# Kernel tuning notes

Measured on AMD Instinct MI355X. Metric: run time of the kernel, lower is better.

Reference implementation:

```python
import jax, jax.numpy as jnp
import numpy as np

B, S, D = 8, 2048, 256


def setup_inputs() -> dict:
    key = jax.random.key(0)
    ks = jax.random.split(key, 8)
    nodes = jax.random.normal(ks[0], (B, S, D), dtype=jnp.float32)
    mask = jax.random.randint(ks[1], (B, S), 0, 2, dtype=jnp.int32)
    # ensure at least one unmasked position per row to avoid all--inf softmax
    mask = mask.at[:, 0].set(1)
    scale = 1.0 / np.sqrt(D)
    Wq = jax.random.normal(ks[2], (D, D), dtype=jnp.float32) * scale
    bq = jnp.zeros((D,), dtype=jnp.float32)
    Wk = jax.random.normal(ks[3], (D, D), dtype=jnp.float32) * scale
    bk = jnp.zeros((D,), dtype=jnp.float32)
    Wv = jax.random.normal(ks[4], (D, D), dtype=jnp.float32) * scale
    bv = jnp.zeros((D,), dtype=jnp.float32)
    return {"nodes": nodes, "mask": mask, "Wq": Wq, "bq": bq,
            "Wk": Wk, "bk": bk, "Wv": Wv, "bv": bv}


def reference(nodes, mask, Wq, bq, Wk, bk, Wv, bv):
    # Linear layers: x @ W.T + b (torch nn.Linear convention)
    q = jnp.einsum('bsd,ed->bse', nodes, Wq) + bq   # [B,S,D]
    k = jnp.einsum('bsd,ed->bse', nodes, Wk) + bk
    v = jnp.einsum('bsd,ed->bse', nodes, Wv) + bv
    d = k.shape[-1]
    scores = jnp.einsum('bqd,bkd->bqk', q, k) / jnp.sqrt(jnp.float32(d))  # [B,S,S]
    # mask[b, j] == 0 masks key column j for every query row
    scores = jnp.where(mask[:, None, :] != 0, scores, -jnp.inf)
    attn = jax.nn.softmax(scores, axis=-1)           # [B,S,S]
    weighted = jnp.einsum('bqk,bkd->bqd', attn, v)   # [B,S,D]
    return jnp.mean(weighted, axis=1)                # [B,D]
```

## Files before the change

### kernel.cpp

```cpp
#include <hip/hip_runtime.h>
#include <hip/hip_bf16.h>
#include <stdint.h>


typedef short short8 __attribute__((ext_vector_type(8)));
typedef float floatx4 __attribute__((ext_vector_type(4)));

#define MFMA16(a, b, c) __builtin_amdgcn_mfma_f32_16x16x32_bf16((a), (b), (c), 0, 0, 0)

static __device__ __forceinline__ unsigned short f2bf(float f) {
    union { float f; unsigned u; } v; v.f = f;
    unsigned r = v.u + 0x7fffu + ((v.u >> 16) & 1u);
    return (unsigned short)(r >> 16);
}
static __device__ __forceinline__ float bf2f(unsigned short h) {
    union { unsigned u; float f; } v; v.u = ((unsigned)h) << 16;
    return v.f;
}

__global__ __launch_bounds__(256) void k_convert(
    const float* __restrict__ nodes, const float* __restrict__ Wq,
    const float* __restrict__ Wk, const float* __restrict__ Wv,
    unsigned short* __restrict__ nbf, unsigned short* __restrict__ wbf)
{
    int unit = blockIdx.x * 256 + threadIdx.x;
    const float* src;
    unsigned short* dst;
    int off;
    if (unit < 524288) {
        src = nodes; dst = nbf; off = unit * 8;
    } else {
        int j = (unit - 524288) * 8;
        int m = j >> 16;
        int r = j & 65535;
        src = (m == 0) ? Wq : (m == 1 ? Wk : Wv);
        dst = wbf + m * 65536;
        off = r;
    }
    float4 a = *(const float4*)(src + off);
    float4 b = *(const float4*)(src + off + 4);
    short8 o;
    o[0] = f2bf(a.x); o[1] = f2bf(a.y); o[2] = f2bf(a.z); o[3] = f2bf(a.w);
    o[4] = f2bf(b.x); o[5] = f2bf(b.y); o[6] = f2bf(b.z); o[7] = f2bf(b.w);
    *(short8*)(dst + off) = o;
}

__global__ __launch_bounds__(256) void k_proj2(
    const unsigned short* __restrict__ nbf,
    const unsigned short* __restrict__ wbf,
    const float* __restrict__ bq, const float* __restrict__ bk,
    const float* __restrict__ bv,
    unsigned short* __restrict__ qb, unsigned short* __restrict__ kb,
    unsigned short* __restrict__ vb)
{
    __shared__ unsigned short As[128 * 64];
    __shared__ unsigned short Bs[128 * 64];
    int tid = threadIdx.x, lane = tid & 63, wave = tid >> 6;
    int wm = wave & 1, wn = wave >> 1;
    int l15 = lane & 15, quad = lane >> 4;
    int mBase = blockIdx.x * 128;
    int nBase = blockIdx.y * 128;
    int z = blockIdx.z;
    const unsigned short* W = wbf + z * 65536;

    floatx4 acc[4][4] = {};

    int srow[4], scol[4];
#pragma unroll
    for (int i = 0; i < 4; ++i) {
        int p = i * 256 + tid;
        srow[i] = p >> 3;
        scol[i] = (p & 7) ^ (srow[i] & 7);
    }

    for (int kc = 0; kc < 256; kc += 64) {
#pragma unroll
        for (int i = 0; i < 4; ++i) {
            int p = i * 256 + tid;
            *(short8*)(&As[p * 8]) =
                *(const short8*)(nbf + (mBase + srow[i]) * 256 + kc + scol[i] * 8);
            *(short8*)(&Bs[p * 8]) =
                *(const short8*)(W + (nBase + srow[i]) * 256 + kc + scol[i] * 8);
        }
        __syncthreads();
#pragma unroll
        for (int ks = 0; ks < 2; ++ks) {
            int c8 = ks * 4 + quad;
            short8 af[4], bfr[4];
#pragma unroll
            for (int i = 0; i < 4; ++i) {
                int row = wm * 64 + i * 16 + l15;
                af[i] = *(const short8*)(&As[(row * 8 + (c8 ^ (row & 7))) * 8]);
            }
#pragma unroll
            for (int i = 0; i < 4; ++i) {
                int row = wn * 64 + i * 16 + l15;
                bfr[i] = *(const short8*)(&Bs[(row * 8 + (c8 ^ (row & 7))) * 8]);
            }
#pragma unroll
            for (int mi = 0; mi < 4; ++mi)
#pragma unroll
                for (int ni = 0; ni < 4; ++ni)
                    acc[mi][ni] = MFMA16(af[mi], bfr[ni], acc[mi][ni]);
        }
        __syncthreads();
    }

    const float* bias = (z == 0) ? bq : (z == 1 ? bk : bv);
    unsigned short* out = (z == 0) ? qb : (z == 1 ? kb : vb);
    float scale = (z == 0) ? 0.0625f : 1.0f;
#pragma unroll
    for (int mi = 0; mi < 4; ++mi)
#pragma unroll
        for (int ni = 0; ni < 4; ++ni) {
            int col = nBase + wn * 64 + ni * 16 + l15;
            float bval = bias[col];
#pragma unroll
            for (int r = 0; r < 4; ++r) {
                int row = mBase + wm * 64 + mi * 16 + quad * 4 + r;
                out[row * 256 + col] = f2bf((acc[mi][ni][r] + bval) * scale);
            }
        }
}

#define LDSW 264

template <bool STORE_P>
__global__ __launch_bounds__(256) void k_pass1(
    const unsigned short* __restrict__ qb, const unsigned short* __restrict__ kb,
    const int* __restrict__ mask, float* __restrict__ lsum_g,
    unsigned short* __restrict__ pbuf)
{
    __shared__ unsigned short kt[64 * LDSW];
    __shared__ float mf[64];
    int tid = threadIdx.x, lane = tid & 63, wave = tid >> 6;
    int l15 = lane & 15, quad = lane >> 4;
    int b = blockIdx.z;
    int qBase = blockIdx.x * 128 + wave * 32;
    int kStart = blockIdx.y * 512;
    _Float16* P = (_Float16*)pbuf;

    short8 qf[2][8];
#pragma unroll
    for (int mi = 0; mi < 2; ++mi)
#pragma unroll
        for (int ks = 0; ks < 8; ++ks)
            qf[mi][ks] = *(const short8*)(qb + (b * 2048 + qBase + mi * 16 + l15) * 256 + ks * 32 + quad * 8);

    float ls[2][4] = {};
    for (int kc = kStart; kc < kStart + 512; kc += 64) {
#pragma unroll
        for (int u = tid; u < 2048; u += 256) {
            int row = u >> 5, cu = u & 31;
            *(uint4*)(&kt[row * LDSW + cu * 8]) = *(const uint4*)(kb + (b * 2048 + kc) * 256 + u * 8);
        }
        if (tid < 64) mf[tid] = mask[b * 2048 + kc + tid] ? 0.0f : -1e30f;
        __syncthreads();
#pragma unroll
        for (int nt = 0; nt < 4; ++nt) {
            short8 kf[8];
            const unsigned short* base = &kt[(nt * 16 + l15) * LDSW + quad * 8];
#pragma unroll
            for (int ks = 0; ks < 8; ++ks) kf[ks] = *(const short8*)(base + ks * 32);
            floatx4 acc[2] = {};
#pragma unroll
            for (int ks = 0; ks < 8; ++ks) {
                acc[0] = MFMA16(qf[0][ks], kf[ks], acc[0]);
                acc[1] = MFMA16(qf[1][ks], kf[ks], acc[1]);
            }
            float bv = mf[nt * 16 + l15];
#pragma unroll
            for (int mi = 0; mi < 2; ++mi)
#pragma unroll
                for (int r = 0; r < 4; ++r) {
                    float e = __expf(acc[mi][r] + bv);
                    ls[mi][r] += e;
                    if (STORE_P) {
                        int q = qBase + mi * 16 + quad * 4 + r;
                        P[(b * 2048 + q) * 2048 + kc + nt * 16 + l15] = (_Float16)e;
                    }
                }
        }
        __syncthreads();
    }
#pragma unroll
    for (int mi = 0; mi < 2; ++mi)
#pragma unroll
        for (int r = 0; r < 4; ++r) {
            float v = ls[mi][r];
            v += __shfl_xor(v, 1); v += __shfl_xor(v, 2);
            v += __shfl_xor(v, 4); v += __shfl_xor(v, 8);
            if (l15 == 0)
                atomicAdd(&lsum_g[b * 2048 + qBase + mi * 16 + quad * 4 + r], v);
        }
}

__global__ __launch_bounds__(256) void k_wred(
    const unsigned short* __restrict__ pbuf, const float* __restrict__ lsum_g,
    float* __restrict__ wsum_g)
{
    int b = blockIdx.z;
    int k = (blockIdx.x * 256 + threadIdx.x) * 2;
    int q0 = blockIdx.y * 128;
    const unsigned short* P = pbuf;
    float a0 = 0.f, a1 = 0.f;
#pragma unroll 8
    for (int q = q0; q < q0 + 128; ++q) {
        float li = 1.0f / lsum_g[b * 2048 + q];
        union { unsigned u; _Float16 h[2]; } v;
        v.u = *(const unsigned*)(P + (b * 2048 + q) * 2048 + k);
        a0 += (float)v.h[0] * li;
        a1 += (float)v.h[1] * li;
    }
    atomicAdd(&wsum_g[b * 2048 + k], a0);
    atomicAdd(&wsum_g[b * 2048 + k + 1], a1);
}

__global__ __launch_bounds__(256) void k_pass2(
    const unsigned short* __restrict__ qb, const unsigned short* __restrict__ kb,
    const int* __restrict__ mask, const float* __restrict__ lsum_g,
    float* __restrict__ wsum_g)
{
    __shared__ unsigned short kt[64 * LDSW];
    __shared__ float mf[64];
    int tid = threadIdx.x, lane = tid & 63, wave = tid >> 6;
    int l15 = lane & 15, quad = lane >> 4;
    int b = blockIdx.z;
    int qBase = blockIdx.x * 128 + wave * 32;
    int kStart = blockIdx.y * 512;

    short8 qf[2][8];
    float linv[2][4];
#pragma unroll
    for (int mi = 0; mi < 2; ++mi) {
#pragma unroll
        for (int ks = 0; ks < 8; ++ks)
            qf[mi][ks] = *(const short8*)(qb + (b * 2048 + qBase + mi * 16 + l15) * 256 + ks * 32 + quad * 8);
#pragma unroll
        for (int r = 0; r < 4; ++r)
            linv[mi][r] = 1.0f / lsum_g[b * 2048 + qBase + mi * 16 + quad * 4 + r];
    }

    for (int kc = kStart; kc < kStart + 512; kc += 64) {
#pragma unroll
        for (int u = tid; u < 2048; u += 256) {
            int row = u >> 5, cu = u & 31;
            *(uint4*)(&kt[row * LDSW + cu * 8]) = *(const uint4*)(kb + (b * 2048 + kc) * 256 + u * 8);
        }
        if (tid < 64) mf[tid] = mask[b * 2048 + kc + tid] ? 1.0f : 0.0f;
        __syncthreads();
#pragma unroll
        for (int nt = 0; nt < 4; ++nt) {
            short8 kf[8];
            const unsigned short* base = &kt[(nt * 16 + l15) * LDSW + quad * 8];
#pragma unroll
            for (int ks = 0; ks < 8; ++ks) kf[ks] = *(const short8*)(base + ks * 32);
            floatx4 acc[2] = {};
#pragma unroll
            for (int ks = 0; ks < 8; ++ks) {
                acc[0] = MFMA16(qf[0][ks], kf[ks], acc[0]);
                acc[1] = MFMA16(qf[1][ks], kf[ks], acc[1]);
            }
            float mv = mf[nt * 16 + l15];
            float part = 0.f;
#pragma unroll
            for (int mi = 0; mi < 2; ++mi)
#pragma unroll
                for (int r = 0; r < 4; ++r)
                    part += mv * __expf(fminf(acc[mi][r], 30.f)) * linv[mi][r];
            part += __shfl_xor(part, 16);
            part += __shfl_xor(part, 32);
            if (lane < 16)
                atomicAdd(&wsum_g[b * 2048 + kc + nt * 16 + lane], part);
        }
        __syncthreads();
    }
}

__global__ __launch_bounds__(256) void k_out(
    const float* __restrict__ wsum_g, const unsigned short* __restrict__ vb,
    float* __restrict__ outp)
{
    int b = blockIdx.y;
    int d = threadIdx.x;
    int k0 = blockIdx.x * 128;
    float acc = 0.f;
#pragma unroll 4
    for (int k = k0; k < k0 + 128; ++k) {
        float wv = wsum_g[b * 2048 + k];
        acc += wv * bf2f(vb[(b * 2048 + k) * 256 + d]);
    }
    atomicAdd(&outp[b * 256 + d], acc * (1.0f / 2048.0f));
}

extern "C" void kernel_launch(void* const* d_in, const int* in_sizes, int n_in,
                              void* d_out, int out_size, void* d_ws, size_t ws_size,
                              hipStream_t stream)
{
    const float* nodes = (const float*)d_in[0];
    const int*   mask  = (const int*)d_in[1];
    const float* Wq    = (const float*)d_in[2];
    const float* bq    = (const float*)d_in[3];
    const float* Wk    = (const float*)d_in[4];
    const float* bk    = (const float*)d_in[5];
    const float* Wv    = (const float*)d_in[6];
    const float* bv    = (const float*)d_in[7];
    float* out = (float*)d_out;

    unsigned short* qb  = (unsigned short*)d_ws;
    unsigned short* kb  = qb + 4194304;
    unsigned short* vb  = kb + 4194304;
    float* lsum = (float*)(vb + 4194304);
    float* wsum = lsum + 16384;
    unsigned short* X   = (unsigned short*)(wsum + 16384);
    unsigned short* nbf = X;
    unsigned short* wbf = X + 4194304;
    unsigned short* pbuf = X;

    bool useP = ws_size >= 92500000;

    hipMemsetAsync(lsum, 0, 16384 * sizeof(float), stream);
    hipMemsetAsync(wsum, 0, 16384 * sizeof(float), stream);
    hipMemsetAsync(d_out, 0, 2048 * sizeof(float), stream);

    k_convert<<<2144, 256, 0, stream>>>(nodes, Wq, Wk, Wv, nbf, wbf);
    k_proj2<<<dim3(128, 2, 3), 256, 0, stream>>>(nbf, wbf, bq, bk, bv, qb, kb, vb);
    if (useP) {
        k_pass1<true><<<dim3(16, 4, 8), 256, 0, stream>>>(qb, kb, mask, lsum, pbuf);
        k_wred<<<dim3(4, 16, 8), 256, 0, stream>>>(pbuf, lsum, wsum);
    } else {
        k_pass1<false><<<dim3(16, 4, 8), 256, 0, stream>>>(qb, kb, mask, lsum, pbuf);
        k_pass2<<<dim3(16, 4, 8), 256, 0, stream>>>(qb, kb, mask, lsum, wsum);
    }
    k_out<<<dim3(16, 8), 256, 0, stream>>>(wsum, vb, out);
}
```

Baseline: 155.9 us.

## Store P in MFMA-tile layout, XOR-swizzle K in LDS, rewrite column reduction

The score kernel now writes exp values as contiguous 16-byte per-lane fragments in an MFMA-tile-ordered buffer instead of scattered 2-byte stores, and the K tile in LDS uses an XOR swizzle instead of padding. The key range per block is halved to launch twice as many blocks. The column-sum kernel is rewritten to read the tiled layout, with per-query inverse sums cached in LDS and a shuffle reduction before the atomic add. The aim is to remove uncoalesced P stores and raise occupancy, at the cost of a custom layout that both kernels must agree on.

```diff
diff --git a/kernel.cpp b/kernel.cpp
--- a/kernel.cpp
+++ b/kernel.cpp
@@ -123,22 +123,19 @@
         }
 }
 
-#define LDSW 264
-
 template <bool STORE_P>
 __global__ __launch_bounds__(256) void k_pass1(
     const unsigned short* __restrict__ qb, const unsigned short* __restrict__ kb,
     const int* __restrict__ mask, float* __restrict__ lsum_g,
     unsigned short* __restrict__ pbuf)
 {
-    __shared__ unsigned short kt[64 * LDSW];
+    __shared__ unsigned short kt[64 * 32 * 8];
     __shared__ float mf[64];
     int tid = threadIdx.x, lane = tid & 63, wave = tid >> 6;
     int l15 = lane & 15, quad = lane >> 4;
     int b = blockIdx.z;
     int qBase = blockIdx.x * 128 + wave * 32;
-    int kStart = blockIdx.y * 512;
-    _Float16* P = (_Float16*)pbuf;
+    int kStart = blockIdx.y * 256;
 
     short8 qf[2][8];
 #pragma unroll
@@ -148,38 +145,47 @@
             qf[mi][ks] = *(const short8*)(qb + (b * 2048 + qBase + mi * 16 + l15) * 256 + ks * 32 + quad * 8);
 
     float ls[2][4] = {};
-    for (int kc = kStart; kc < kStart + 512; kc += 64) {
+    for (int kc = kStart; kc < kStart + 256; kc += 64) {
 #pragma unroll
         for (int u = tid; u < 2048; u += 256) {
             int row = u >> 5, cu = u & 31;
-            *(uint4*)(&kt[row * LDSW + cu * 8]) = *(const uint4*)(kb + (b * 2048 + kc) * 256 + u * 8);
+            int slot = row * 32 + (cu ^ (row & 7));
+            *(uint4*)(&kt[slot * 8]) = *(const uint4*)(kb + (b * 2048 + kc) * 256 + u * 8);
         }
         if (tid < 64) mf[tid] = mask[b * 2048 + kc + tid] ? 0.0f : -1e30f;
         __syncthreads();
 #pragma unroll
         for (int nt = 0; nt < 4; ++nt) {
+            int row = nt * 16 + l15;
             short8 kf[8];
-            const unsigned short* base = &kt[(nt * 16 + l15) * LDSW + quad * 8];
-#pragma unroll
-            for (int ks = 0; ks < 8; ++ks) kf[ks] = *(const short8*)(base + ks * 32);
+#pragma unroll
+            for (int ks = 0; ks < 8; ++ks) {
+                int c8 = ks * 4 + quad;
+                kf[ks] = *(const short8*)(&kt[(row * 32 + (c8 ^ (row & 7))) * 8]);
+            }
             floatx4 acc[2] = {};
 #pragma unroll
             for (int ks = 0; ks < 8; ++ks) {
                 acc[0] = MFMA16(qf[0][ks], kf[ks], acc[0]);
                 acc[1] = MFMA16(qf[1][ks], kf[ks], acc[1]);
             }
-            float bv = mf[nt * 16 + l15];
+            float bvv = mf[row];
+            short8 hh;
 #pragma unroll
             for (int mi = 0; mi < 2; ++mi)
 #pragma unroll
                 for (int r = 0; r < 4; ++r) {
-                    float e = __expf(acc[mi][r] + bv);
+                    float e = __expf(acc[mi][r] + bvv);
                     ls[mi][r] += e;
                     if (STORE_P) {
-                        int q = qBase + mi * 16 + quad * 4 + r;
-                        P[(b * 2048 + q) * 2048 + kc + nt * 16 + l15] = (_Float16)e;
+                        union { _Float16 h; short s; } u; u.h = (_Float16)e;
+                        hh[mi * 4 + r] = u.s;
                     }
                 }
+            if (STORE_P) {
+                size_t tileIdx = ((((size_t)b * 16 + blockIdx.x) * 4 + wave) * 32 + (kc >> 6)) * 4 + nt;
+                *(short8*)(pbuf + tileIdx * 512 + lane * 8) = hh;
+            }
         }
         __syncthreads();
     }
@@ -195,27 +201,43 @@
         }
 }
 
-__global__ __launch_bounds__(256) void k_wred(
+__global__ __launch_bounds__(512) void k_wred2(
     const unsigned short* __restrict__ pbuf, const float* __restrict__ lsum_g,
     float* __restrict__ wsum_g)
 {
-    int b = blockIdx.z;
-    int k = (blockIdx.x * 256 + threadIdx.x) * 2;
-    int q0 = blockIdx.y * 128;
-    const unsigned short* P = pbuf;
-    float a0 = 0.f, a1 = 0.f;
-#pragma unroll 8
-    for (int q = q0; q < q0 + 128; ++q) {
-        float li = 1.0f / lsum_g[b * 2048 + q];
-        union { unsigned u; _Float16 h[2]; } v;
-        v.u = *(const unsigned*)(P + (b * 2048 + q) * 2048 + k);
-        a0 += (float)v.h[0] * li;
-        a1 += (float)v.h[1] * li;
-    }
-    atomicAdd(&wsum_g[b * 2048 + k], a0);
-    atomicAdd(&wsum_g[b * 2048 + k + 1], a1);
-}
-
+    __shared__ float linv_s[2048];
+    int tid = threadIdx.x, lane = tid & 63, wave = tid >> 6;
+    int l15 = lane & 15, quad = lane >> 4;
+    int b = blockIdx.y, kc = blockIdx.x;
+    int nt = wave & 3;
+    int qg0 = (wave >> 2) * 32;
+
+    for (int idx = tid; idx < 2048; idx += 512) {
+        int qg = idx >> 5, qd = (idx >> 3) & 3, j = idx & 7;
+        int q = qg * 32 + (j >> 2) * 16 + qd * 4 + (j & 3);
+        linv_s[idx] = 1.0f / lsum_g[b * 2048 + q];
+    }
+    __syncthreads();
+
+    float acc = 0.f;
+#pragma unroll 4
+    for (int qg = qg0; qg < qg0 + 32; ++qg) {
+        size_t tileIdx = ((((size_t)b * 16 + (qg >> 2)) * 4 + (qg & 3)) * 32 + kc) * 4 + nt;
+        short8 hv = *(const short8*)(pbuf + tileIdx * 512 + lane * 8);
+        const float* lv = &linv_s[(qg * 4 + quad) * 8];
+#pragma unroll
+        for (int j = 0; j < 8; ++j) {
+            union { short s; _Float16 h; } u; u.s = hv[j];
+            acc += (float)u.h * lv[j];
+        }
+    }
+    acc += __shfl_xor(acc, 16);
+    acc += __shfl_xor(acc, 32);
+    if (lane < 16)
+        atomicAdd(&wsum_g[b * 2048 + kc * 64 + nt * 16 + l15], acc);
+}
+
+#define LDSW 264
 __global__ __launch_bounds__(256) void k_pass2(
     const unsigned short* __restrict__ qb, const unsigned short* __restrict__ kb,
     const int* __restrict__ mask, const float* __restrict__ lsum_g,
@@ -326,10 +348,10 @@
     k_convert<<<2144, 256, 0, stream>>>(nodes, Wq, Wk, Wv, nbf, wbf);
     k_proj2<<<dim3(128, 2, 3), 256, 0, stream>>>(nbf, wbf, bq, bk, bv, qb, kb, vb);
     if (useP) {
-        k_pass1<true><<<dim3(16, 4, 8), 256, 0, stream>>>(qb, kb, mask, lsum, pbuf);
-        k_wred<<<dim3(4, 16, 8), 256, 0, stream>>>(pbuf, lsum, wsum);
+        k_pass1<true><<<dim3(16, 8, 8), 256, 0, stream>>>(qb, kb, mask, lsum, pbuf);
+        k_wred2<<<dim3(32, 8), 512, 0, stream>>>(pbuf, lsum, wsum);
     } else {
-        k_pass1<false><<<dim3(16, 4, 8), 256, 0, stream>>>(qb, kb, mask, lsum, pbuf);
+        k_pass1<false><<<dim3(16, 8, 8), 256, 0, stream>>>(qb, kb, mask, lsum, pbuf);
         k_pass2<<<dim3(16, 4, 8), 256, 0, stream>>>(qb, kb, mask, lsum, wsum);
     }
     k_out<<<dim3(16, 8), 256, 0, stream>>>(wsum, vb, out);
```

After: 163.1 us. 1.05x slower.

## Fuse fp32-to-bf16 conversion into projection and restructure attention with tiled P layout

Applied to the files above, without the earlier changes.

Removes the separate conversion kernel by converting fp32 inputs to bf16 inside the projection GEMM's shared-memory staging. Rewrites the score pass so each wave keeps its K tile in registers and streams Q rows, storing exp-scores in an MFMA-fragment-tiled fp16 layout with vectorized 16-byte writes. The scattered per-element 2-byte stores of the old layout go away. A new reduction kernel reads that tiled layout with vector loads and per-block cached inverse row sums. The workspace-size fallback path is dropped, so the P buffer is always used, and lsum now takes more atomics per query row.

```diff
diff --git a/kernel.cpp b/kernel.cpp
--- a/kernel.cpp
+++ b/kernel.cpp
@@ -17,37 +17,17 @@
     union { unsigned u; float f; } v; v.u = ((unsigned)h) << 16;
     return v.f;
 }
-
-__global__ __launch_bounds__(256) void k_convert(
-    const float* __restrict__ nodes, const float* __restrict__ Wq,
-    const float* __restrict__ Wk, const float* __restrict__ Wv,
-    unsigned short* __restrict__ nbf, unsigned short* __restrict__ wbf)
-{
-    int unit = blockIdx.x * 256 + threadIdx.x;
-    const float* src;
-    unsigned short* dst;
-    int off;
-    if (unit < 524288) {
-        src = nodes; dst = nbf; off = unit * 8;
-    } else {
-        int j = (unit - 524288) * 8;
-        int m = j >> 16;
-        int r = j & 65535;
-        src = (m == 0) ? Wq : (m == 1 ? Wk : Wv);
-        dst = wbf + m * 65536;
-        off = r;
-    }
-    float4 a = *(const float4*)(src + off);
-    float4 b = *(const float4*)(src + off + 4);
+static __device__ __forceinline__ short8 cvt8(float4 a, float4 b) {
     short8 o;
     o[0] = f2bf(a.x); o[1] = f2bf(a.y); o[2] = f2bf(a.z); o[3] = f2bf(a.w);
     o[4] = f2bf(b.x); o[5] = f2bf(b.y); o[6] = f2bf(b.z); o[7] = f2bf(b.w);
-    *(short8*)(dst + off) = o;
-}
-
-__global__ __launch_bounds__(256) void k_proj2(
-    const unsigned short* __restrict__ nbf,
-    const unsigned short* __restrict__ wbf,
+    return o;
+}
+
+__global__ __launch_bounds__(256) void k_proj3(
+    const float* __restrict__ nodes,
+    const float* __restrict__ Wq, const float* __restrict__ Wk,
+    const float* __restrict__ Wv,
     const float* __restrict__ bq, const float* __restrict__ bk,
     const float* __restrict__ bv,
     unsigned short* __restrict__ qb, unsigned short* __restrict__ kb,
@@ -61,7 +41,7 @@
     int mBase = blockIdx.x * 128;
     int nBase = blockIdx.y * 128;
     int z = blockIdx.z;
-    const unsigned short* W = wbf + z * 65536;
+    const float* W = (z == 0) ? Wq : (z == 1 ? Wk : Wv);
 
     floatx4 acc[4][4] = {};
 
@@ -77,10 +57,10 @@
 #pragma unroll
         for (int i = 0; i < 4; ++i) {
             int p = i * 256 + tid;
-            *(short8*)(&As[p * 8]) =
-                *(const short8*)(nbf + (mBase + srow[i]) * 256 + kc + scol[i] * 8);
-            *(short8*)(&Bs[p * 8]) =
-                *(const short8*)(W + (nBase + srow[i]) * 256 + kc + scol[i] * 8);
+            const float* ap = nodes + (mBase + srow[i]) * 256 + kc + scol[i] * 8;
+            const float* bp = W + (nBase + srow[i]) * 256 + kc + scol[i] * 8;
+            *(short8*)(&As[p * 8]) = cvt8(*(const float4*)ap, *(const float4*)(ap + 4));
+            *(short8*)(&Bs[p * 8]) = cvt8(*(const float4*)bp, *(const float4*)(bp + 4));
         }
         __syncthreads();
 #pragma unroll
@@ -123,158 +103,123 @@
         }
 }
 
-#define LDSW 264
-
-template <bool STORE_P>
-__global__ __launch_bounds__(256) void k_pass1(
+__global__ __launch_bounds__(256, 2) void k_attn(
     const unsigned short* __restrict__ qb, const unsigned short* __restrict__ kb,
     const int* __restrict__ mask, float* __restrict__ lsum_g,
     unsigned short* __restrict__ pbuf)
 {
-    __shared__ unsigned short kt[64 * LDSW];
-    __shared__ float mf[64];
     int tid = threadIdx.x, lane = tid & 63, wave = tid >> 6;
     int l15 = lane & 15, quad = lane >> 4;
     int b = blockIdx.z;
-    int qBase = blockIdx.x * 128 + wave * 32;
-    int kStart = blockIdx.y * 512;
-    _Float16* P = (_Float16*)pbuf;
-
-    short8 qf[2][8];
-#pragma unroll
-    for (int mi = 0; mi < 2; ++mi)
+    int kbase = blockIdx.x * 128 + wave * 32;
+    int qs = blockIdx.y * 256;
+
+    short8 kf[2][8];
+    float mb[2];
+#pragma unroll
+    for (int nt = 0; nt < 2; ++nt) {
+        int krow = b * 2048 + kbase + nt * 16 + l15;
 #pragma unroll
         for (int ks = 0; ks < 8; ++ks)
-            qf[mi][ks] = *(const short8*)(qb + (b * 2048 + qBase + mi * 16 + l15) * 256 + ks * 32 + quad * 8);
-
-    float ls[2][4] = {};
-    for (int kc = kStart; kc < kStart + 512; kc += 64) {
-#pragma unroll
-        for (int u = tid; u < 2048; u += 256) {
-            int row = u >> 5, cu = u & 31;
-            *(uint4*)(&kt[row * LDSW + cu * 8]) = *(const uint4*)(kb + (b * 2048 + kc) * 256 + u * 8);
-        }
-        if (tid < 64) mf[tid] = mask[b * 2048 + kc + tid] ? 0.0f : -1e30f;
-        __syncthreads();
-#pragma unroll
-        for (int nt = 0; nt < 4; ++nt) {
-            short8 kf[8];
-            const unsigned short* base = &kt[(nt * 16 + l15) * LDSW + quad * 8];
-#pragma unroll
-            for (int ks = 0; ks < 8; ++ks) kf[ks] = *(const short8*)(base + ks * 32);
-            floatx4 acc[2] = {};
-#pragma unroll
-            for (int ks = 0; ks < 8; ++ks) {
-                acc[0] = MFMA16(qf[0][ks], kf[ks], acc[0]);
-                acc[1] = MFMA16(qf[1][ks], kf[ks], acc[1]);
-            }
-            float bv = mf[nt * 16 + l15];
+            kf[nt][ks] = *(const short8*)(kb + krow * 256 + ks * 32 + quad * 8);
+        mb[nt] = mask[b * 2048 + kbase + nt * 16 + l15] ? 0.0f : -1e30f;
+    }
+
+    for (int qc = 0; qc < 8; ++qc) {
+        int qBase = qs + qc * 32;
+        short8 af[2][8];
+#pragma unroll
+        for (int mi = 0; mi < 2; ++mi) {
+            int qrow = b * 2048 + qBase + mi * 16 + l15;
+#pragma unroll
+            for (int ks = 0; ks < 8; ++ks)
+                af[mi][ks] = *(const short8*)(qb + qrow * 256 + ks * 32 + quad * 8);
+        }
+        floatx4 acc[2][2] = {};
+#pragma unroll
+        for (int ks = 0; ks < 8; ++ks) {
+            acc[0][0] = MFMA16(af[0][ks], kf[0][ks], acc[0][0]);
+            acc[0][1] = MFMA16(af[0][ks], kf[1][ks], acc[0][1]);
+            acc[1][0] = MFMA16(af[1][ks], kf[0][ks], acc[1][0]);
+            acc[1][1] = MFMA16(af[1][ks], kf[1][ks], acc[1][1]);
+        }
+        float e[2][2][4];
+#pragma unroll
+        for (int mi = 0; mi < 2; ++mi)
+#pragma unroll
+            for (int nt = 0; nt < 2; ++nt)
+#pragma unroll
+                for (int r = 0; r < 4; ++r)
+                    e[mi][nt][r] = __expf(acc[mi][nt][r] + mb[nt]);
+
+        int qcg = blockIdx.y * 8 + qc;
+#pragma unroll
+        for (int nt = 0; nt < 2; ++nt) {
+            short8 hh;
 #pragma unroll
             for (int mi = 0; mi < 2; ++mi)
 #pragma unroll
                 for (int r = 0; r < 4; ++r) {
-                    float e = __expf(acc[mi][r] + bv);
-                    ls[mi][r] += e;
-                    if (STORE_P) {
-                        int q = qBase + mi * 16 + quad * 4 + r;
-                        P[(b * 2048 + q) * 2048 + kc + nt * 16 + l15] = (_Float16)e;
-                    }
+                    union { _Float16 h; short s; } u;
+                    u.h = (_Float16)e[mi][nt][r];
+                    hh[mi * 4 + r] = u.s;
                 }
-        }
-        __syncthreads();
-    }
-#pragma unroll
-    for (int mi = 0; mi < 2; ++mi)
-#pragma unroll
-        for (int r = 0; r < 4; ++r) {
-            float v = ls[mi][r];
-            v += __shfl_xor(v, 1); v += __shfl_xor(v, 2);
-            v += __shfl_xor(v, 4); v += __shfl_xor(v, 8);
-            if (l15 == 0)
-                atomicAdd(&lsum_g[b * 2048 + qBase + mi * 16 + quad * 4 + r], v);
-        }
-}
-
-__global__ __launch_bounds__(256) void k_wred(
+            int ktile = blockIdx.x * 8 + wave * 2 + nt;
+            size_t off = ((((size_t)b * 128 + ktile) * 64 + qcg) * 64 + lane) * 8;
+            *(short8*)(pbuf + off) = hh;
+        }
+#pragma unroll
+        for (int mi = 0; mi < 2; ++mi)
+#pragma unroll
+            for (int r = 0; r < 4; ++r) {
+                float v = e[mi][0][r] + e[mi][1][r];
+                v += __shfl_xor(v, 1); v += __shfl_xor(v, 2);
+                v += __shfl_xor(v, 4); v += __shfl_xor(v, 8);
+                if (l15 == 0)
+                    atomicAdd(&lsum_g[b * 2048 + qBase + mi * 16 + quad * 4 + r], v);
+            }
+    }
+}
+
+__global__ __launch_bounds__(512) void k_wred3(
     const unsigned short* __restrict__ pbuf, const float* __restrict__ lsum_g,
     float* __restrict__ wsum_g)
 {
-    int b = blockIdx.z;
-    int k = (blockIdx.x * 256 + threadIdx.x) * 2;
-    int q0 = blockIdx.y * 128;
-    const unsigned short* P = pbuf;
-    float a0 = 0.f, a1 = 0.f;
-#pragma unroll 8
-    for (int q = q0; q < q0 + 128; ++q) {
-        float li = 1.0f / lsum_g[b * 2048 + q];
-        union { unsigned u; _Float16 h[2]; } v;
-        v.u = *(const unsigned*)(P + (b * 2048 + q) * 2048 + k);
-        a0 += (float)v.h[0] * li;
-        a1 += (float)v.h[1] * li;
-    }
-    atomicAdd(&wsum_g[b * 2048 + k], a0);
-    atomicAdd(&wsum_g[b * 2048 + k + 1], a1);
-}
-
-__global__ __launch_bounds__(256) void k_pass2(
-    const unsigned short* __restrict__ qb, const unsigned short* __restrict__ kb,
-    const int* __restrict__ mask, const float* __restrict__ lsum_g,
-    float* __restrict__ wsum_g)
-{
-    __shared__ unsigned short kt[64 * LDSW];
-    __shared__ float mf[64];
+    __shared__ float linv_p[2048];
     int tid = threadIdx.x, lane = tid & 63, wave = tid >> 6;
     int l15 = lane & 15, quad = lane >> 4;
     int b = blockIdx.z;
-    int qBase = blockIdx.x * 128 + wave * 32;
-    int kStart = blockIdx.y * 512;
-
-    short8 qf[2][8];
-    float linv[2][4];
-#pragma unroll
-    for (int mi = 0; mi < 2; ++mi) {
-#pragma unroll
-        for (int ks = 0; ks < 8; ++ks)
-            qf[mi][ks] = *(const short8*)(qb + (b * 2048 + qBase + mi * 16 + l15) * 256 + ks * 32 + quad * 8);
-#pragma unroll
-        for (int r = 0; r < 4; ++r)
-            linv[mi][r] = 1.0f / lsum_g[b * 2048 + qBase + mi * 16 + quad * 4 + r];
-    }
-
-    for (int kc = kStart; kc < kStart + 512; kc += 64) {
-#pragma unroll
-        for (int u = tid; u < 2048; u += 256) {
-            int row = u >> 5, cu = u & 31;
-            *(uint4*)(&kt[row * LDSW + cu * 8]) = *(const uint4*)(kb + (b * 2048 + kc) * 256 + u * 8);
-        }
-        if (tid < 64) mf[tid] = mask[b * 2048 + kc + tid] ? 1.0f : 0.0f;
-        __syncthreads();
-#pragma unroll
-        for (int nt = 0; nt < 4; ++nt) {
-            short8 kf[8];
-            const unsigned short* base = &kt[(nt * 16 + l15) * LDSW + quad * 8];
-#pragma unroll
-            for (int ks = 0; ks < 8; ++ks) kf[ks] = *(const short8*)(base + ks * 32);
-            floatx4 acc[2] = {};
-#pragma unroll
-            for (int ks = 0; ks < 8; ++ks) {
-                acc[0] = MFMA16(qf[0][ks], kf[ks], acc[0]);
-                acc[1] = MFMA16(qf[1][ks], kf[ks], acc[1]);
-            }
-            float mv = mf[nt * 16 + l15];
-            float part = 0.f;
-#pragma unroll
-            for (int mi = 0; mi < 2; ++mi)
-#pragma unroll
-                for (int r = 0; r < 4; ++r)
-                    part += mv * __expf(fminf(acc[mi][r], 30.f)) * linv[mi][r];
-            part += __shfl_xor(part, 16);
-            part += __shfl_xor(part, 32);
-            if (lane < 16)
-                atomicAdd(&wsum_g[b * 2048 + kc + nt * 16 + lane], part);
-        }
-        __syncthreads();
-    }
+    int ktile = blockIdx.y * 8 + wave;
+
+#pragma unroll
+    for (int i = 0; i < 4; ++i) {
+        int idx = i * 512 + tid;
+        int qcg = idx >> 5, qd = (idx >> 3) & 3, j = idx & 7;
+        int q = qcg * 32 + (j >> 2) * 16 + qd * 4 + (j & 3);
+        linv_p[idx] = 1.0f / lsum_g[b * 2048 + q];
+    }
+    __syncthreads();
+
+    int qcg0 = blockIdx.x * 32;
+    float acc = 0.f;
+#pragma unroll 4
+    for (int qcg = qcg0; qcg < qcg0 + 32; ++qcg) {
+        size_t off = ((((size_t)b * 128 + ktile) * 64 + qcg) * 64 + lane) * 8;
+        short8 pv = *(const short8*)(pbuf + off);
+        const float* lv = &linv_p[(qcg * 4 + quad) * 8];
+        floatx4 l0 = *(const floatx4*)lv;
+        floatx4 l1 = *(const floatx4*)(lv + 4);
+#pragma unroll
+        for (int j = 0; j < 4; ++j) {
+            union { short s; _Float16 h; } u0, u1;
+            u0.s = pv[j]; u1.s = pv[4 + j];
+            acc += (float)u0.h * l0[j] + (float)u1.h * l1[j];
+        }
+    }
+    acc += __shfl_xor(acc, 16);
+    acc += __shfl_xor(acc, 32);
+    if (lane < 16)
+        atomicAdd(&wsum_g[b * 2048 + ktile * 16 + l15], acc);
 }
 
 __global__ __launch_bounds__(256) void k_out(
@@ -312,25 +257,15 @@
     unsigned short* vb  = kb + 4194304;
     float* lsum = (float*)(vb + 4194304);
     float* wsum = lsum + 16384;
-    unsigned short* X   = (unsigned short*)(wsum + 16384);
-    unsigned short* nbf = X;
-    unsigned short* wbf = X + 4194304;
-    unsigned short* pbuf = X;
-
-    bool useP = ws_size >= 92500000;
+    unsigned short* pbuf = (unsigned short*)(wsum + 16384);
 
     hipMemsetAsync(lsum, 0, 16384 * sizeof(float), stream);
     hipMemsetAsync(wsum, 0, 16384 * sizeof(float), stream);
     hipMemsetAsync(d_out, 0, 2048 * sizeof(float), stream);
 
-    k_convert<<<2144, 256, 0, stream>>>(nodes, Wq, Wk, Wv, nbf, wbf);
-    k_proj2<<<dim3(128, 2, 3), 256, 0, stream>>>(nbf, wbf, bq, bk, bv, qb, kb, vb);
-    if (useP) {
-        k_pass1<true><<<dim3(16, 4, 8), 256, 0, stream>>>(qb, kb, mask, lsum, pbuf);
-        k_wred<<<dim3(4, 16, 8), 256, 0, stream>>>(pbuf, lsum, wsum);
-    } else {
-        k_pass1<false><<<dim3(16, 4, 8), 256, 0, stream>>>(qb, kb, mask, lsum, pbuf);
-        k_pass2<<<dim3(16, 4, 8), 256, 0, stream>>>(qb, kb, mask, lsum, wsum);
-    }
+    k_proj3<<<dim3(128, 2, 3), 256, 0, stream>>>(nodes, Wq, Wk, Wv, bq, bk, bv,
+                                                 qb, kb, vb);
+    k_attn<<<dim3(16, 8, 8), 256, 0, stream>>>(qb, kb, mask, lsum, pbuf);
+    k_wred3<<<dim3(2, 16, 8), 512, 0, stream>>>(pbuf, lsum, wsum);
     k_out<<<dim3(16, 8), 256, 0, stream>>>(wsum, vb, out);
 }
```

New measurement: 194.9 us. 1.25x slower.

## Compact unmasked keys and fuse bf16 conversion into projection

Applied to the files above, without the earlier changes.

Adds a per-batch compaction kernel that gathers the indices of unmasked keys, and the two attention passes now iterate only over that compacted key list, skipping the fully masked columns. The fp32-to-bf16 conversion moves inside the projection GEMM's shared-memory load, so the separate conversion kernel and its scratch buffer go away. The P-buffer store/reduce path is dropped in favour of always recomputing scores in pass 2. Keys are gathered indirectly into an XOR-swizzled LDS layout, and the grid is widened to 8 key-slices that stride over the compacted range.

```diff
diff --git a/kernel.cpp b/kernel.cpp
--- a/kernel.cpp
+++ b/kernel.cpp
@@ -17,37 +17,33 @@
     union { unsigned u; float f; } v; v.u = ((unsigned)h) << 16;
     return v.f;
 }
-
-__global__ __launch_bounds__(256) void k_convert(
-    const float* __restrict__ nodes, const float* __restrict__ Wq,
-    const float* __restrict__ Wk, const float* __restrict__ Wv,
-    unsigned short* __restrict__ nbf, unsigned short* __restrict__ wbf)
-{
-    int unit = blockIdx.x * 256 + threadIdx.x;
-    const float* src;
-    unsigned short* dst;
-    int off;
-    if (unit < 524288) {
-        src = nodes; dst = nbf; off = unit * 8;
-    } else {
-        int j = (unit - 524288) * 8;
-        int m = j >> 16;
-        int r = j & 65535;
-        src = (m == 0) ? Wq : (m == 1 ? Wk : Wv);
-        dst = wbf + m * 65536;
-        off = r;
-    }
-    float4 a = *(const float4*)(src + off);
-    float4 b = *(const float4*)(src + off + 4);
+static __device__ __forceinline__ short8 cvt8(float4 a, float4 b) {
     short8 o;
     o[0] = f2bf(a.x); o[1] = f2bf(a.y); o[2] = f2bf(a.z); o[3] = f2bf(a.w);
     o[4] = f2bf(b.x); o[5] = f2bf(b.y); o[6] = f2bf(b.z); o[7] = f2bf(b.w);
-    *(short8*)(dst + off) = o;
-}
-
-__global__ __launch_bounds__(256) void k_proj2(
-    const unsigned short* __restrict__ nbf,
-    const unsigned short* __restrict__ wbf,
+    return o;
+}
+
+__global__ __launch_bounds__(64) void k_compact(
+    const int* __restrict__ mask, int* __restrict__ cidx, int* __restrict__ cnt)
+{
+    int b = blockIdx.x, lane = threadIdx.x;
+    int base = 0;
+    for (int c = 0; c < 2048; c += 64) {
+        int m = mask[b * 2048 + c + lane];
+        unsigned long long bal = __ballot(m != 0);
+        int pre = __popcll(bal & ((1ull << lane) - 1ull));
+        if (m) cidx[b * 2048 + base + pre] = c + lane;
+        base += __popcll(bal);
+    }
+    if (lane == 0) cnt[b] = base;
+    for (int i = base + lane; i < 2048; i += 64) cidx[b * 2048 + i] = 0;
+}
+
+__global__ __launch_bounds__(256) void k_proj3(
+    const float* __restrict__ nodes,
+    const float* __restrict__ Wq, const float* __restrict__ Wk,
+    const float* __restrict__ Wv,
     const float* __restrict__ bq, const float* __restrict__ bk,
     const float* __restrict__ bv,
     unsigned short* __restrict__ qb, unsigned short* __restrict__ kb,
@@ -61,7 +57,7 @@
     int mBase = blockIdx.x * 128;
     int nBase = blockIdx.y * 128;
     int z = blockIdx.z;
-    const unsigned short* W = wbf + z * 65536;
+    const float* W = (z == 0) ? Wq : (z == 1 ? Wk : Wv);
 
     floatx4 acc[4][4] = {};
 
@@ -77,10 +73,10 @@
 #pragma unroll
         for (int i = 0; i < 4; ++i) {
             int p = i * 256 + tid;
-            *(short8*)(&As[p * 8]) =
-                *(const short8*)(nbf + (mBase + srow[i]) * 256 + kc + scol[i] * 8);
-            *(short8*)(&Bs[p * 8]) =
-                *(const short8*)(W + (nBase + srow[i]) * 256 + kc + scol[i] * 8);
+            const float* ap = nodes + (mBase + srow[i]) * 256 + kc + scol[i] * 8;
+            const float* bp = W + (nBase + srow[i]) * 256 + kc + scol[i] * 8;
+            *(short8*)(&As[p * 8]) = cvt8(*(const float4*)ap, *(const float4*)(ap + 4));
+            *(short8*)(&Bs[p * 8]) = cvt8(*(const float4*)bp, *(const float4*)(bp + 4));
         }
         __syncthreads();
 #pragma unroll
@@ -123,22 +119,19 @@
         }
 }
 
-#define LDSW 264
-
-template <bool STORE_P>
-__global__ __launch_bounds__(256) void k_pass1(
+__global__ __launch_bounds__(256) void k_pass1c(
     const unsigned short* __restrict__ qb, const unsigned short* __restrict__ kb,
-    const int* __restrict__ mask, float* __restrict__ lsum_g,
-    unsigned short* __restrict__ pbuf)
-{
-    __shared__ unsigned short kt[64 * LDSW];
+    const int* __restrict__ cidx, const int* __restrict__ cnt_g,
+    float* __restrict__ lsum_g)
+{
+    __shared__ unsigned short kt[64 * 32 * 8];
     __shared__ float mf[64];
     int tid = threadIdx.x, lane = tid & 63, wave = tid >> 6;
     int l15 = lane & 15, quad = lane >> 4;
     int b = blockIdx.z;
     int qBase = blockIdx.x * 128 + wave * 32;
-    int kStart = blockIdx.y * 512;
-    _Float16* P = (_Float16*)pbuf;
+    int cnt = cnt_g[b];
+    int cntPad = (cnt + 63) & ~63;
 
     short8 qf[2][8];
 #pragma unroll
@@ -148,38 +141,37 @@
             qf[mi][ks] = *(const short8*)(qb + (b * 2048 + qBase + mi * 16 + l15) * 256 + ks * 32 + quad * 8);
 
     float ls[2][4] = {};
-    for (int kc = kStart; kc < kStart + 512; kc += 64) {
+    for (int kc = blockIdx.y * 64; kc < cntPad; kc += 512) {
 #pragma unroll
         for (int u = tid; u < 2048; u += 256) {
             int row = u >> 5, cu = u & 31;
-            *(uint4*)(&kt[row * LDSW + cu * 8]) = *(const uint4*)(kb + (b * 2048 + kc) * 256 + u * 8);
-        }
-        if (tid < 64) mf[tid] = mask[b * 2048 + kc + tid] ? 0.0f : -1e30f;
+            int krow = cidx[b * 2048 + kc + row];
+            int slot = row * 32 + (cu ^ (row & 7));
+            *(uint4*)(&kt[slot * 8]) = *(const uint4*)(kb + (b * 2048 + krow) * 256 + cu * 8);
+        }
+        if (tid < 64) mf[tid] = (kc + tid < cnt) ? 0.0f : -1e30f;
         __syncthreads();
 #pragma unroll
         for (int nt = 0; nt < 4; ++nt) {
+            int row = nt * 16 + l15;
             short8 kf[8];
-            const unsigned short* base = &kt[(nt * 16 + l15) * LDSW + quad * 8];
-#pragma unroll
-            for (int ks = 0; ks < 8; ++ks) kf[ks] = *(const short8*)(base + ks * 32);
+#pragma unroll
+            for (int ks = 0; ks < 8; ++ks) {
+                int c8 = ks * 4 + quad;
+                kf[ks] = *(const short8*)(&kt[(row * 32 + (c8 ^ (row & 7))) * 8]);
+            }
             floatx4 acc[2] = {};
 #pragma unroll
             for (int ks = 0; ks < 8; ++ks) {
                 acc[0] = MFMA16(qf[0][ks], kf[ks], acc[0]);
                 acc[1] = MFMA16(qf[1][ks], kf[ks], acc[1]);
             }
-            float bv = mf[nt * 16 + l15];
+            float bvv = mf[row];
 #pragma unroll
             for (int mi = 0; mi < 2; ++mi)
 #pragma unroll
-                for (int r = 0; r < 4; ++r) {
-                    float e = __expf(acc[mi][r] + bv);
-                    ls[mi][r] += e;
-                    if (STORE_P) {
-                        int q = qBase + mi * 16 + quad * 4 + r;
-                        P[(b * 2048 + q) * 2048 + kc + nt * 16 + l15] = (_Float16)e;
-                    }
-                }
+                for (int r = 0; r < 4; ++r)
+                    ls[mi][r] += __expf(acc[mi][r] + bvv);
         }
         __syncthreads();
     }
@@ -195,39 +187,19 @@
         }
 }
 
-__global__ __launch_bounds__(256) void k_wred(
-    const unsigned short* __restrict__ pbuf, const float* __restrict__ lsum_g,
-    float* __restrict__ wsum_g)
-{
-    int b = blockIdx.z;
-    int k = (blockIdx.x * 256 + threadIdx.x) * 2;
-    int q0 = blockIdx.y * 128;
-    const unsigned short* P = pbuf;
-    float a0 = 0.f, a1 = 0.f;
-#pragma unroll 8
-    for (int q = q0; q < q0 + 128; ++q) {
-        float li = 1.0f / lsum_g[b * 2048 + q];
-        union { unsigned u; _Float16 h[2]; } v;
-        v.u = *(const unsigned*)(P + (b * 2048 + q) * 2048 + k);
-        a0 += (float)v.h[0] * li;
-        a1 += (float)v.h[1] * li;
-    }
-    atomicAdd(&wsum_g[b * 2048 + k], a0);
-    atomicAdd(&wsum_g[b * 2048 + k + 1], a1);
-}
-
-__global__ __launch_bounds__(256) void k_pass2(
+__global__ __launch_bounds__(256) void k_pass2c(
     const unsigned short* __restrict__ qb, const unsigned short* __restrict__ kb,
-    const int* __restrict__ mask, const float* __restrict__ lsum_g,
-    float* __restrict__ wsum_g)
-{
-    __shared__ unsigned short kt[64 * LDSW];
+    const int* __restrict__ cidx, const int* __restrict__ cnt_g,
+    const float* __restrict__ lsum_g, float* __restrict__ wsum_g)
+{
+    __shared__ unsigned short kt[64 * 32 * 8];
     __shared__ float mf[64];
     int tid = threadIdx.x, lane = tid & 63, wave = tid >> 6;
     int l15 = lane & 15, quad = lane >> 4;
     int b = blockIdx.z;
     int qBase = blockIdx.x * 128 + wave * 32;
-    int kStart = blockIdx.y * 512;
+    int cnt = cnt_g[b];
+    int cntPad = (cnt + 63) & ~63;
 
     short8 qf[2][8];
     float linv[2][4];
@@ -241,37 +213,44 @@
             linv[mi][r] = 1.0f / lsum_g[b * 2048 + qBase + mi * 16 + quad * 4 + r];
     }
 
-    for (int kc = kStart; kc < kStart + 512; kc += 64) {
+    for (int kc = blockIdx.y * 64; kc < cntPad; kc += 512) {
 #pragma unroll
         for (int u = tid; u < 2048; u += 256) {
             int row = u >> 5, cu = u & 31;
-            *(uint4*)(&kt[row * LDSW + cu * 8]) = *(const uint4*)(kb + (b * 2048 + kc) * 256 + u * 8);
-        }
-        if (tid < 64) mf[tid] = mask[b * 2048 + kc + tid] ? 1.0f : 0.0f;
+            int krow = cidx[b * 2048 + kc + row];
+            int slot = row * 32 + (cu ^ (row & 7));
+            *(uint4*)(&kt[slot * 8]) = *(const uint4*)(kb + (b * 2048 + krow) * 256 + cu * 8);
+        }
+        if (tid < 64) mf[tid] = (kc + tid < cnt) ? 0.0f : -1e30f;
         __syncthreads();
 #pragma unroll
         for (int nt = 0; nt < 4; ++nt) {
+            int row = nt * 16 + l15;
             short8 kf[8];
-            const unsigned short* base = &kt[(nt * 16 + l15) * LDSW + quad * 8];
-#pragma unroll
-            for (int ks = 0; ks < 8; ++ks) kf[ks] = *(const short8*)(base + ks * 32);
+#pragma unroll
+            for (int ks = 0; ks < 8; ++ks) {
+                int c8 = ks * 4 + quad;
+                kf[ks] = *(const short8*)(&kt[(row * 32 + (c8 ^ (row & 7))) * 8]);
+            }
             floatx4 acc[2] = {};
 #pragma unroll
             for (int ks = 0; ks < 8; ++ks) {
                 acc[0] = MFMA16(qf[0][ks], kf[ks], acc[0]);
                 acc[1] = MFMA16(qf[1][ks], kf[ks], acc[1]);
             }
-            float mv = mf[nt * 16 + l15];
+            float bvv = mf[row];
             float part = 0.f;
 #pragma unroll
             for (int mi = 0; mi < 2; ++mi)
 #pragma unroll
                 for (int r = 0; r < 4; ++r)
-                    part += mv * __expf(fminf(acc[mi][r], 30.f)) * linv[mi][r];
+                    part += __expf(acc[mi][r] + bvv) * linv[mi][r];
             part += __shfl_xor(part, 16);
             part += __shfl_xor(part, 32);
-            if (lane < 16)
-                atomicAdd(&wsum_g[b * 2048 + kc + nt * 16 + lane], part);
+            if (lane < 16) {
+                int key = cidx[b * 2048 + kc + nt * 16 + l15];
+                atomicAdd(&wsum_g[b * 2048 + key], part);
+            }
         }
         __syncthreads();
     }
@@ -312,25 +291,17 @@
     unsigned short* vb  = kb + 4194304;
     float* lsum = (float*)(vb + 4194304);
     float* wsum = lsum + 16384;
-    unsigned short* X   = (unsigned short*)(wsum + 16384);
-    unsigned short* nbf = X;
-    unsigned short* wbf = X + 4194304;
-    unsigned short* pbuf = X;
-
-    bool useP = ws_size >= 92500000;
+    int*   cnt  = (int*)(wsum + 16384);
+    int*   cidx = cnt + 16;
 
     hipMemsetAsync(lsum, 0, 16384 * sizeof(float), stream);
     hipMemsetAsync(wsum, 0, 16384 * sizeof(float), stream);
     hipMemsetAsync(d_out, 0, 2048 * sizeof(float), stream);
 
-    k_convert<<<2144, 256, 0, stream>>>(nodes, Wq, Wk, Wv, nbf, wbf);
-    k_proj2<<<dim3(128, 2, 3), 256, 0, stream>>>(nbf, wbf, bq, bk, bv, qb, kb, vb);
-    if (useP) {
-        k_pass1<true><<<dim3(16, 4, 8), 256, 0, stream>>>(qb, kb, mask, lsum, pbuf);
-        k_wred<<<dim3(4, 16, 8), 256, 0, stream>>>(pbuf, lsum, wsum);
-    } else {
-        k_pass1<false><<<dim3(16, 4, 8), 256, 0, stream>>>(qb, kb, mask, lsum, pbuf);
-        k_pass2<<<dim3(16, 4, 8), 256, 0, stream>>>(qb, kb, mask, lsum, wsum);
-    }
+    k_compact<<<8, 64, 0, stream>>>(mask, cidx, cnt);
+    k_proj3<<<dim3(128, 2, 3), 256, 0, stream>>>(nodes, Wq, Wk, Wv, bq, bk, bv,
+                                                 qb, kb, vb);
+    k_pass1c<<<dim3(16, 8, 8), 256, 0, stream>>>(qb, kb, cidx, cnt, lsum);
+    k_pass2c<<<dim3(16, 8, 8), 256, 0, stream>>>(qb, kb, cidx, cnt, lsum, wsum);
     k_out<<<dim3(16, 8), 256, 0, stream>>>(wsum, vb, out);
 }
```

Measured after the change: 246.7 us. 1.58x slower.
